# Performance work log

Hardware: AMD Instinct MI355X
Metric: run time of the kernel (lower is better)

The kernel has to match this reference:

```python
import jax, jax.numpy as jnp
import numpy as np

N = 4096      # num_nodes (single graph; batch is all-zeros in the original when absent)
CIN = 1024    # in_channels
H = 1024      # hidden_channels
COUT = 512    # out_channels
R = 10        # nodevec rank (hardcoded in the module)
BN_EPS = 1e-5


def setup_inputs() -> dict:
    key = jax.random.key(0)
    ks = jax.random.split(key, 8)
    w = lambda k, shp: jax.random.normal(k, shp, dtype=jnp.float32) * 0.02
    return {
        "x": jax.random.normal(ks[0], (N, CIN), dtype=jnp.float32),
        "w_map": w(ks[1], (CIN, H)),
        "b_map": jnp.zeros((H,), jnp.float32),
        "nv1": jax.random.normal(ks[2], (N, R), dtype=jnp.float32),
        "nv2": jax.random.normal(ks[3], (R, N), dtype=jnp.float32),
        "w1": w(ks[4], (H, H)),
        "b1": jnp.zeros((H,), jnp.float32),
        "w2": w(ks[5], (H, COUT)),
        "b2": jnp.zeros((COUT,), jnp.float32),
        "bn1_g": jnp.ones((H,), jnp.float32),
        "bn1_b": jnp.zeros((H,), jnp.float32),
        "bn1_m": jnp.zeros((H,), jnp.float32),
        "bn1_v": jnp.ones((H,), jnp.float32),
        "bn2_g": jnp.ones((COUT,), jnp.float32),
        "bn2_b": jnp.zeros((COUT,), jnp.float32),
        "bn2_m": jnp.zeros((COUT,), jnp.float32),
        "bn2_v": jnp.ones((COUT,), jnp.float32),
        "w_attn": w(ks[6], (COUT, 1)),
        "b_attn": jnp.zeros((1,), jnp.float32),
    }


def _batchnorm_eval(h, g, b, m, v):
    # BatchNorm1d in eval mode: running stats
    return (h - m) * jax.lax.rsqrt(v + BN_EPS) * g + b


def reference(x, w_map, b_map, nv1, nv2, w1, b1, w2, b2,
              bn1_g, bn1_b, bn1_m, bn1_v, bn2_g, bn2_b, bn2_m, bn2_v,
              w_attn, b_attn):
    # feature mapping
    xm = jax.nn.relu(x @ w_map + b_map)                       # [N, H]
    # adaptive adjacency: softmax(relu(nv1 @ nv2), dim=1) -> strictly positive,
    # so nonzero() yields the fully dense edge list; we keep it dense.
    adp = jax.nn.softmax(jax.nn.relu(nv1 @ nv2), axis=1)      # [N, N]
    # gcn_norm (PyG GCNConv default): add unit self-loops, normalize by
    # column-degree^-1/2 on both sides.
    A = adp + jnp.eye(N, dtype=adp.dtype)                      # [N, N]
    deg = jnp.sum(A, axis=0)                                   # column sums (target degree)
    dinv = jnp.where(deg > 0, jax.lax.rsqrt(deg), 0.0)
    An = (dinv[:, None] * A) * dinv[None, :]                   # D^-1/2 A D^-1/2
    # GCNConv: out_i = sum_j An[j, i] * (x W)_j + bias  =>  An^T @ (X W) + b
    h = jax.nn.relu(An.T @ (xm @ w1) + b1)                     # conv1 + relu
    h = _batchnorm_eval(h, bn1_g, bn1_b, bn1_m, bn1_v)         # bn1 (dropout off in eval)
    h = jax.nn.relu(An.T @ (h @ w2) + b2)                      # conv2 + relu
    h = _batchnorm_eval(h, bn2_g, bn2_b, bn2_m, bn2_v)         # bn2
    # global_mean_pool with batch == zeros -> single-graph mean
    pooled = jnp.mean(h, axis=0, keepdims=True)                # [1, COUT]
    attn = jax.nn.sigmoid(pooled @ w_attn + b_attn)            # [1, 1]
    return pooled * attn                                       # [1, COUT]
```

## Files before the change

kernel.cpp:

```cpp
#include <hip/hip_runtime.h>

#define NN 4096
#define R_RANK 10

typedef __bf16 bf16x8 __attribute__((ext_vector_type(8)));
typedef float floatx4 __attribute__((ext_vector_type(4)));

__device__ __forceinline__ unsigned short f2bf(float f) {
    union { float f; unsigned int u; } v; v.f = f;
    unsigned int r = v.u + 0x7FFFu + ((v.u >> 16) & 1u);
    return (unsigned short)(r >> 16);
}
__device__ __forceinline__ void gll16(const void* g, void* l) {
    __builtin_amdgcn_global_load_lds(
        (const __attribute__((address_space(1))) unsigned int*)g,
        (__attribute__((address_space(3))) unsigned int*)l, 16, 0, 0);
}

__global__ __launch_bounds__(256) void row_stats_kernel(
    const float* __restrict__ nv1, const float* __restrict__ nv2,
    float* __restrict__ rowmax, float* __restrict__ rowsum,
    float* __restrict__ deg, float* __restrict__ pooled)
{
    const int i0 = blockIdx.x * 4;
    const int tid = threadIdx.x;
    if (blockIdx.x < 16) deg[blockIdx.x * 256 + tid] = 0.f;
    if (blockIdx.x >= 16 && blockIdx.x < 18) pooled[(blockIdx.x - 16) * 256 + tid] = 0.f;
    __shared__ float a[4][R_RANK];
    if (tid < 4 * R_RANK) a[tid / R_RANK][tid % R_RANK] = nv1[i0 * R_RANK + tid];
    __syncthreads();

    float s[4][16];
    float mx[4] = {0.f, 0.f, 0.f, 0.f};
    #pragma unroll
    for (int t = 0; t < 16; ++t) {
        const int j = t * 256 + tid;
        float v[R_RANK];
        #pragma unroll
        for (int r = 0; r < R_RANK; ++r) v[r] = nv2[r * NN + j];
        #pragma unroll
        for (int q = 0; q < 4; ++q) {
            float acc = 0.f;
            #pragma unroll
            for (int r = 0; r < R_RANK; ++r) acc = fmaf(a[q][r], v[r], acc);
            acc = fmaxf(acc, 0.f);
            s[q][t] = acc;
            mx[q] = fmaxf(mx[q], acc);
        }
    }
    __shared__ float red[4][4];
    #pragma unroll
    for (int q = 0; q < 4; ++q) {
        float m = mx[q];
        #pragma unroll
        for (int off = 32; off > 0; off >>= 1) m = fmaxf(m, __shfl_down(m, off, 64));
        if ((tid & 63) == 0) red[q][tid >> 6] = m;
    }
    __syncthreads();
    #pragma unroll
    for (int q = 0; q < 4; ++q)
        mx[q] = fmaxf(fmaxf(red[q][0], red[q][1]), fmaxf(red[q][2], red[q][3]));
    __syncthreads();
    float sm[4] = {0.f, 0.f, 0.f, 0.f};
    #pragma unroll
    for (int t = 0; t < 16; ++t)
        #pragma unroll
        for (int q = 0; q < 4; ++q) sm[q] += __expf(s[q][t] - mx[q]);
    #pragma unroll
    for (int q = 0; q < 4; ++q) {
        float m = sm[q];
        #pragma unroll
        for (int off = 32; off > 0; off >>= 1) m += __shfl_down(m, off, 64);
        if ((tid & 63) == 0) red[q][tid >> 6] = m;
    }
    __syncthreads();
    if (tid < 4) {
        rowmax[i0 + tid] = mx[tid];
        rowsum[i0 + tid] = red[tid][0] + red[tid][1] + red[tid][2] + red[tid][3];
    }
}

__global__ __launch_bounds__(256) void col_sum_kernel(
    const float* __restrict__ nv1, const float* __restrict__ nv2,
    const float* __restrict__ rowmax, const float* __restrict__ rowsum,
    float* __restrict__ deg)
{
    const int j = blockIdx.x * 256 + threadIdx.x;
    const int i0 = blockIdx.y * 256;
    float v[R_RANK];
    #pragma unroll
    for (int r = 0; r < R_RANK; ++r) v[r] = nv2[r * NN + j];
    float acc = 0.f;
    for (int i = i0; i < i0 + 256; ++i) {
        float s = 0.f;
        #pragma unroll
        for (int r = 0; r < R_RANK; ++r) s = fmaf(nv1[i * R_RANK + r], v[r], s);
        s = fmaxf(s, 0.f);
        acc += __expf(s - rowmax[i]) * (1.0f / rowsum[i]);
    }
    atomicAdd(&deg[j], acc);
}

__global__ __launch_bounds__(256) void an_build_kernel(
    const float* __restrict__ nv1, const float* __restrict__ nv2,
    const float* __restrict__ rowmax, const float* __restrict__ rowsum,
    const float* __restrict__ deg, unsigned short* __restrict__ AnT)
{
    const int tid = threadIdx.x;
    const int j = blockIdx.x * 256 + tid;
    const int i0 = blockIdx.y * 8;
    __shared__ float v2s[8][R_RANK];
    __shared__ float dis[8];
    if (tid < 8 * R_RANK) {
        const int r = tid / 8, t = tid % 8;
        v2s[t][r] = nv2[r * NN + i0 + t];
    }
    if (tid < 8) dis[tid] = rsqrtf(1.0f + deg[i0 + tid]);

    float a[R_RANK];
    #pragma unroll
    for (int r = 0; r < R_RANK; ++r) a[r] = nv1[j * R_RANK + r];
    const float rm = rowmax[j];
    const float rs = 1.0f / rowsum[j];
    const float dj = rsqrtf(1.0f + deg[j]);
    __syncthreads();

    #pragma unroll
    for (int t = 0; t < 8; ++t) {
        const int i = i0 + t;
        float s = 0.f;
        #pragma unroll
        for (int r = 0; r < R_RANK; ++r) s = fmaf(a[r], v2s[t][r], s);
        s = fmaxf(s, 0.f);
        const float adp = __expf(s - rm) * rs;
        const float val = (adp + ((i == j) ? 1.f : 0.f)) * dis[t] * dj;
        AnT[(size_t)i * NN + j] = f2bf(val);
    }
}

__global__ __launch_bounds__(256) void prep_kernel(
    const float* __restrict__ x, const float* __restrict__ w_map,
    const float* __restrict__ w1, const float* __restrict__ w2,
    unsigned short* __restrict__ xb, unsigned short* __restrict__ wmT,
    unsigned short* __restrict__ w1T, unsigned short* __restrict__ w2T)
{
    const int z = blockIdx.z;
    const int tid = threadIdx.x;
    if (z == 3) {
        const int b = blockIdx.x + blockIdx.y * 32;
        const size_t base = (size_t)b * 4096 + (size_t)tid * 16;
        #pragma unroll
        for (int i = 0; i < 2; ++i) {
            const float4 a0 = *(const float4*)(x + base + i * 8);
            const float4 a1 = *(const float4*)(x + base + i * 8 + 4);
            ushort4 p, q;
            p.x = f2bf(a0.x); p.y = f2bf(a0.y); p.z = f2bf(a0.z); p.w = f2bf(a0.w);
            q.x = f2bf(a1.x); q.y = f2bf(a1.y); q.z = f2bf(a1.z); q.w = f2bf(a1.w);
            *(ushort4*)(xb + base + i * 8) = p;
            *(ushort4*)(xb + base + i * 8 + 4) = q;
        }
        return;
    }
    const float* W = (z == 0) ? w_map : (z == 1) ? w1 : w2;
    unsigned short* WT = (z == 0) ? wmT : (z == 1) ? w1T : w2T;
    const int CN = (z == 2) ? 512 : 1024;
    if (blockIdx.x * 32 >= CN) return;
    __shared__ float s[32][33];
    const int tx = tid & 31, ty = tid >> 5;
    const int r0 = blockIdx.y * 32, c0 = blockIdx.x * 32;
    #pragma unroll
    for (int i = 0; i < 4; ++i)
        s[ty + 8 * i][tx] = W[(size_t)(r0 + ty + 8 * i) * CN + c0 + tx];
    __syncthreads();
    #pragma unroll
    for (int i = 0; i < 4; ++i)
        WT[(size_t)(c0 + ty + 8 * i) * 1024 + r0 + tx] = f2bf(s[tx][ty + 8 * i]);
}

template<int OUTM, int EPI, int SK>
__global__ __launch_bounds__(512) void gemm_mfma(
    const unsigned short* __restrict__ A, const unsigned short* __restrict__ Bt,
    void* __restrict__ Out, const int M, const int N, const int K,
    const float* __restrict__ bias, const float* __restrict__ gamma,
    const float* __restrict__ beta, const float* __restrict__ mean,
    const float* __restrict__ var)
{
    __shared__ __align__(16) unsigned short As[4][8192];
    __shared__ __align__(16) unsigned short Bs[4][8192];
    const int tid = threadIdx.x;
    const int l = tid & 63, w = tid >> 6;
    const int wy = w >> 2, wx = w & 3;
    const int lr = l & 15, lq = l >> 4;

    const int gx = gridDim.x, gy = gridDim.y;
    int lin = blockIdx.x + gx * (blockIdx.y + gy * blockIdx.z);
    const int q = (gx * gy * gridDim.z) >> 3;
    lin = (lin & 7) * q + (lin >> 3);
    const int bx = lin % gx;
    const int by = (lin / gx) % gy;
    const int bz = lin / (gx * gy);

    const int row0 = by * 128, col0 = bx * 128;
    const int Kc = K / SK;
    const int kb = bz * Kc;
    const int nt = Kc >> 6;

    const unsigned short* Ag0 = A + (size_t)(row0 + w * 16 + lr) * K + kb + lq * 8;
    const unsigned short* Bg0 = Bt + (size_t)(col0 + w * 16 + lr) * K + kb + lq * 8;

    floatx4 acc[4][2];
    #pragma unroll
    for (int i = 0; i < 4; ++i)
        #pragma unroll
        for (int j = 0; j < 2; ++j) acc[i][j] = (floatx4){0.f, 0.f, 0.f, 0.f};

    #define STAGE(b, t)                                                         \
    {                                                                           \
        char* Aw = (char*)As[b] + w * 1024;                                     \
        char* Bw = (char*)Bs[b] + w * 1024;                                     \
        const int kk = (t) * 64;                                                \
        gll16(Ag0 + kk,      Aw);                                               \
        gll16(Ag0 + kk + 32, Aw + 8192);                                        \
        gll16(Bg0 + kk,      Bw);                                               \
        gll16(Bg0 + kk + 32, Bw + 8192);                                        \
    }

    STAGE(0, 0)
    STAGE(1, 1)
    const int nt2 = nt - 2;
    for (int t = 0; t < nt; ++t) {
        if (t < nt2) {
            STAGE((t + 2) & 3, t + 2)
            asm volatile("s_waitcnt vmcnt(8)" ::: "memory");
        } else if (t == nt2) {
            asm volatile("s_waitcnt vmcnt(4)" ::: "memory");
        } else {
            asm volatile("s_waitcnt vmcnt(0)" ::: "memory");
        }
        __builtin_amdgcn_sched_barrier(0);
        __builtin_amdgcn_s_barrier();
        __builtin_amdgcn_sched_barrier(0);

        const char* Afr = (const char*)As[t & 3] + wy * 4096 + l * 16;
        const char* Bfr = (const char*)Bs[t & 3] + wx * 2048 + l * 16;
        #pragma unroll
        for (int h = 0; h < 2; ++h) {
            bf16x8 af[4], bf[2];
            #pragma unroll
            for (int i = 0; i < 4; ++i) af[i] = *(const bf16x8*)(Afr + h * 8192 + i * 1024);
            #pragma unroll
            for (int j = 0; j < 2; ++j) bf[j] = *(const bf16x8*)(Bfr + h * 8192 + j * 1024);
            #pragma unroll
            for (int mf = 0; mf < 4; ++mf)
                #pragma unroll
                for (int nf = 0; nf < 2; ++nf)
                    acc[mf][nf] = __builtin_amdgcn_mfma_f32_16x16x32_bf16(
                        af[mf], bf[nf], acc[mf][nf], 0, 0, 0);
        }
    }
    #undef STAGE

    const int gr0 = row0 + wy * 64 + lq * 4;
    const int gc0 = col0 + wx * 32 + lr;
    if constexpr (OUTM == 0) {
        float* Pz = (float*)Out + (size_t)bz * M * N;
        #pragma unroll
        for (int mf = 0; mf < 4; ++mf) {
            const int gr = gr0 + mf * 16;
            #pragma unroll
            for (int nf = 0; nf < 2; ++nf) {
                const int gc = gc0 + nf * 16;
                #pragma unroll
                for (int r = 0; r < 4; ++r)
                    Pz[(size_t)(gr + r) * N + gc] = acc[mf][nf][r];
            }
        }
    } else if constexpr (OUTM == 1) {
        unsigned short* O = (unsigned short*)Out;
        #pragma unroll
        for (int nf = 0; nf < 2; ++nf) {
            const int gc = gc0 + nf * 16;
            float bb = 0.f, sc = 1.f, sh = 0.f;
            if constexpr (EPI >= 1) bb = bias[gc];
            if constexpr (EPI == 2) {
                sc = gamma[gc] * rsqrtf(var[gc] + 1e-5f);
                sh = beta[gc] - mean[gc] * sc;
            }
            #pragma unroll
            for (int mf = 0; mf < 4; ++mf) {
                const int gr = gr0 + mf * 16;
                #pragma unroll
                for (int r = 0; r < 4; ++r) {
                    float xv = acc[mf][nf][r];
                    if constexpr (EPI >= 1) xv = fmaxf(xv + bb, 0.f);
                    if constexpr (EPI == 2) xv = fmaf(xv, sc, sh);
                    O[(size_t)(gr + r) * N + gc] = f2bf(xv);
                }
            }
        }
    } else {
        unsigned short* O = (unsigned short*)Out;
        #pragma unroll
        for (int mf = 0; mf < 4; ++mf) {
            const int gr = gr0 + mf * 16;
            #pragma unroll
            for (int nf = 0; nf < 2; ++nf) {
                const int gc = gc0 + nf * 16;
                ushort4 p;
                p.x = f2bf(acc[mf][nf][0]); p.y = f2bf(acc[mf][nf][1]);
                p.z = f2bf(acc[mf][nf][2]); p.w = f2bf(acc[mf][nf][3]);
                *(ushort4*)&O[(size_t)gc * M + gr] = p;
            }
        }
    }
}

template<int EPI, int S, int NC>
__global__ __launch_bounds__(256) void reduce_k(
    const float* __restrict__ P, unsigned short* __restrict__ out, const int MN,
    const float* __restrict__ bias, const float* __restrict__ gamma,
    const float* __restrict__ beta, const float* __restrict__ mean,
    const float* __restrict__ var)
{
    const int idx = blockIdx.x * 256 + threadIdx.x;
    const int n4 = MN >> 2;
    const float4* Pv = (const float4*)P;
    float4 v = Pv[idx];
    #pragma unroll
    for (int z = 1; z < S; ++z) {
        const float4 t = Pv[idx + (size_t)z * n4];
        v.x += t.x; v.y += t.y; v.z += t.z; v.w += t.w;
    }
    float vals[4] = {v.x, v.y, v.z, v.w};
    if constexpr (EPI >= 1) {
        const int c0 = (idx << 2) & (NC - 1);
        const float4 b4 = *(const float4*)(bias + c0);
        const float bb[4] = {b4.x, b4.y, b4.z, b4.w};
        float sc[4], sh[4];
        if constexpr (EPI == 2) {
            const float4 g4 = *(const float4*)(gamma + c0);
            const float4 e4 = *(const float4*)(beta + c0);
            const float4 m4 = *(const float4*)(mean + c0);
            const float4 v4 = *(const float4*)(var + c0);
            const float gg[4] = {g4.x, g4.y, g4.z, g4.w};
            const float ee[4] = {e4.x, e4.y, e4.z, e4.w};
            const float mm[4] = {m4.x, m4.y, m4.z, m4.w};
            const float vv[4] = {v4.x, v4.y, v4.z, v4.w};
            #pragma unroll
            for (int j = 0; j < 4; ++j) {
                sc[j] = gg[j] * rsqrtf(vv[j] + 1e-5f);
                sh[j] = ee[j] - mm[j] * sc[j];
            }
        }
        #pragma unroll
        for (int j = 0; j < 4; ++j) {
            float xv = fmaxf(vals[j] + bb[j], 0.f);
            if constexpr (EPI == 2) xv = fmaf(xv, sc[j], sh[j]);
            vals[j] = xv;
        }
    }
    ushort4 p;
    p.x = f2bf(vals[0]); p.y = f2bf(vals[1]); p.z = f2bf(vals[2]); p.w = f2bf(vals[3]);
    *(ushort4*)(out + ((size_t)idx << 2)) = p;
}

template<int S>
__global__ __launch_bounds__(256) void reduce_pool_kernel(
    const float* __restrict__ P, float* __restrict__ pooled,
    const float* __restrict__ bias, const float* __restrict__ gamma,
    const float* __restrict__ beta, const float* __restrict__ mean,
    const float* __restrict__ var)
{
    const int idx = blockIdx.x * 256 + threadIdx.x;
    const int row = blockIdx.x >> 2;
    constexpr int n4 = 512 * 4096 / 4;
    const float4* Pv = (const float4*)P;
    float4 v = Pv[idx];
    #pragma unroll
    for (int z = 1; z < S; ++z) {
        const float4 t = Pv[idx + (size_t)z * n4];
        v.x += t.x; v.y += t.y; v.z += t.z; v.w += t.w;
    }
    const float b0 = bias[row];
    const float sc = gamma[row] * rsqrtf(var[row] + 1e-5f);
    const float sh = beta[row] - mean[row] * sc;
    float s = 0.f;
    const float vals[4] = {v.x, v.y, v.z, v.w};
    #pragma unroll
    for (int j = 0; j < 4; ++j)
        s += fmaf(fmaxf(vals[j] + b0, 0.f), sc, sh);
    #pragma unroll
    for (int off = 32; off > 0; off >>= 1) s += __shfl_down(s, off, 64);
    __shared__ float red[4];
    if ((threadIdx.x & 63) == 0) red[threadIdx.x >> 6] = s;
    __syncthreads();
    if (threadIdx.x == 0)
        atomicAdd(&pooled[row], red[0] + red[1] + red[2] + red[3]);
}

__global__ __launch_bounds__(512) void finalize_kernel(
    const float* __restrict__ pooled, const float* __restrict__ w_attn,
    const float* __restrict__ b_attn, float* __restrict__ out)
{
    const int c = threadIdx.x;
    __shared__ float red[512];
    const float p = pooled[c] * (1.0f / 4096.0f);
    red[c] = p * w_attn[c];
    __syncthreads();
    for (int s = 256; s > 0; s >>= 1) {
        if (c < s) red[c] += red[c + s];
        __syncthreads();
    }
    const float attn = 1.0f / (1.0f + __expf(-(red[0] + b_attn[0])));
    out[c] = p * attn;
}

extern "C" void kernel_launch(void* const* d_in, const int* in_sizes, int n_in,
                              void* d_out, int out_size, void* d_ws, size_t ws_size,
                              hipStream_t stream) {
    const float* x      = (const float*)d_in[0];
    const float* w_map  = (const float*)d_in[1];
    const float* b_map  = (const float*)d_in[2];
    const float* nv1    = (const float*)d_in[3];
    const float* nv2    = (const float*)d_in[4];
    const float* w1     = (const float*)d_in[5];
    const float* b1     = (const float*)d_in[6];
    const float* w2     = (const float*)d_in[7];
    const float* b2     = (const float*)d_in[8];
    const float* bn1_g  = (const float*)d_in[9];
    const float* bn1_b  = (const float*)d_in[10];
    const float* bn1_m  = (const float*)d_in[11];
    const float* bn1_v  = (const float*)d_in[12];
    const float* bn2_g  = (const float*)d_in[13];
    const float* bn2_b  = (const float*)d_in[14];
    const float* bn2_m  = (const float*)d_in[15];
    const float* bn2_v  = (const float*)d_in[16];
    const float* w_attn = (const float*)d_in[17];
    const float* b_attn = (const float*)d_in[18];
    float* out = (float*)d_out;

    const size_t MB = 1024 * 1024;
    char* ws = (char*)d_ws;
    unsigned short* AnT = (unsigned short*)(ws);
    float*          P   = (float*)(ws + 32 * MB);
    char* B0 = ws + 64 * MB;
    unsigned short* xb  = (unsigned short*)(B0);
    unsigned short* t1T = (unsigned short*)(B0);
    unsigned short* t2T = (unsigned short*)(B0);
    unsigned short* xm  = (unsigned short*)(B0 + 8 * MB);
    unsigned short* h1  = (unsigned short*)(B0 + 8 * MB);
    unsigned short* wmT = (unsigned short*)(B0 + 16 * MB);
    unsigned short* w1T = (unsigned short*)(B0 + 18 * MB);
    unsigned short* w2T = (unsigned short*)(B0 + 20 * MB);
    float* deg    = (float*)(B0 + 21 * MB);
    float* rowmax = deg + 4096;
    float* rowsum = rowmax + 4096;
    float* pooled = rowsum + 4096;

    prep_kernel<<<dim3(32, 32, 4), 256, 0, stream>>>(x, w_map, w1, w2, xb, wmT, w1T, w2T);
    row_stats_kernel<<<1024, 256, 0, stream>>>(nv1, nv2, rowmax, rowsum, deg, pooled);
    col_sum_kernel<<<dim3(16, 16), 256, 0, stream>>>(nv1, nv2, rowmax, rowsum, deg);
    an_build_kernel<<<dim3(16, 512), 256, 0, stream>>>(nv1, nv2, rowmax, rowsum, deg, AnT);

    gemm_mfma<1, 1, 1><<<dim3(8, 32, 1), 512, 0, stream>>>(xb, wmT, xm,
        4096, 1024, 1024, b_map, nullptr, nullptr, nullptr, nullptr);
    gemm_mfma<2, 0, 1><<<dim3(8, 32, 1), 512, 0, stream>>>(xm, w1T, t1T,
        4096, 1024, 1024, nullptr, nullptr, nullptr, nullptr, nullptr);
    gemm_mfma<1, 2, 1><<<dim3(8, 32, 1), 512, 0, stream>>>(AnT, t1T, h1,
        4096, 1024, 4096, b1, bn1_g, bn1_b, bn1_m, bn1_v);
    gemm_mfma<0, 0, 2><<<dim3(32, 4, 2), 512, 0, stream>>>(w2T, h1, P,
        512, 4096, 1024, nullptr, nullptr, nullptr, nullptr, nullptr);
    reduce_k<0, 2, 1><<<2048, 256, 0, stream>>>(P, t2T, 2097152,
        nullptr, nullptr, nullptr, nullptr, nullptr);
    gemm_mfma<0, 0, 2><<<dim3(32, 4, 2), 512, 0, stream>>>(t2T, AnT, P,
        512, 4096, 4096, nullptr, nullptr, nullptr, nullptr, nullptr);
    reduce_pool_kernel<2><<<2048, 256, 0, stream>>>(
        P, pooled, b2, bn2_g, bn2_b, bn2_m, bn2_v);

    finalize_kernel<<<1, 512, 0, stream>>>(pooled, w_attn, b_attn, out);
}
```

Before: 356.3 us.

## Add 256x256-tile split-K MFMA GEMM for the adjacency aggregations

Adds a new bf16 MFMA GEMM kernel with 256x256 output tiles, a 64-wide K step, double-buffered LDS loads via global_load_lds, a remapped block order and split-K partials written as fp32. Both An^T aggregation GEMMs now use it, followed by reduce kernels that apply bias, ReLU and batchnorm (or pooling) over the partials. The xm@w1 GEMM is recast to produce the transposed output directly instead of using a transposed-store epilogue. The larger tiles raise data reuse per block and split-K keeps the grid filled. The cost is extra fp32 partial traffic and reduction passes, plus a workspace-size-dependent choice between 4-way and 2-way split.

Result: slower. 368.0 us (+3.3%).

```diff
diff --git a/kernel.cpp b/kernel.cpp
--- a/kernel.cpp
+++ b/kernel.cpp
@@ -275,7 +275,7 @@
                     Pz[(size_t)(gr + r) * N + gc] = acc[mf][nf][r];
             }
         }
-    } else if constexpr (OUTM == 1) {
+    } else {
         unsigned short* O = (unsigned short*)Out;
         #pragma unroll
         for (int nf = 0; nf < 2; ++nf) {
@@ -298,19 +298,108 @@
                 }
             }
         }
-    } else {
-        unsigned short* O = (unsigned short*)Out;
-        #pragma unroll
-        for (int mf = 0; mf < 4; ++mf) {
-            const int gr = gr0 + mf * 16;
-            #pragma unroll
-            for (int nf = 0; nf < 2; ++nf) {
-                const int gc = gc0 + nf * 16;
-                ushort4 p;
-                p.x = f2bf(acc[mf][nf][0]); p.y = f2bf(acc[mf][nf][1]);
-                p.z = f2bf(acc[mf][nf][2]); p.w = f2bf(acc[mf][nf][3]);
-                *(ushort4*)&O[(size_t)gc * M + gr] = p;
-            }
+    }
+}
+
+template<int SK>
+__global__ __launch_bounds__(512, 2) void gemm_mfma256(
+    const unsigned short* __restrict__ A, const unsigned short* __restrict__ Bt,
+    float* __restrict__ P, const int M, const int N, const int K)
+{
+    __shared__ __align__(16) unsigned short L[2][32768];
+    const int tid = threadIdx.x;
+    const int l = tid & 63, w = tid >> 6;
+    const int wy = w >> 2, wx = w & 3;
+    const int lr = l & 15, lq = l >> 4;
+    (void)lr; (void)lq;
+
+    const int gx = gridDim.x, gy = gridDim.y;
+    int lin = blockIdx.x + gx * (blockIdx.y + gy * blockIdx.z);
+    const int q = (gx * gy * gridDim.z) >> 3;
+    lin = (lin & 7) * q + (lin >> 3);
+    const int bx = lin % gx;
+    const int by = (lin / gx) % gy;
+    const int bz = lin / (gx * gy);
+
+    const int row0 = by * 256, col0 = bx * 256;
+    const int Kc = K / SK, kb = bz * Kc;
+    const int nt = Kc >> 6;
+
+    const unsigned short* Ag0 = A + (size_t)(row0 + 32 * w + (l & 15)) * K + kb + (l >> 4) * 8;
+    const unsigned short* Ag1 = Ag0 + (size_t)16 * K;
+    const unsigned short* Bg0 = Bt + (size_t)(col0 + 32 * w + (l & 15)) * K + kb + (l >> 4) * 8;
+    const unsigned short* Bg1 = Bg0 + (size_t)16 * K;
+
+    floatx4 acc[8][4];
+    #pragma unroll
+    for (int i = 0; i < 8; ++i)
+        #pragma unroll
+        for (int j = 0; j < 4; ++j) acc[i][j] = (floatx4){0.f, 0.f, 0.f, 0.f};
+
+    #define STAGE256(b, t)                                                      \
+    {                                                                           \
+        char* Ld = (char*)L[b] + w * 2048;                                      \
+        const int kk = (t) * 64;                                                \
+        gll16(Ag0 + kk,      Ld);                                               \
+        gll16(Ag1 + kk,      Ld + 1024);                                        \
+        gll16(Ag0 + kk + 32, Ld + 16384);                                       \
+        gll16(Ag1 + kk + 32, Ld + 16384 + 1024);                                \
+        gll16(Bg0 + kk,      Ld + 32768);                                       \
+        gll16(Bg1 + kk,      Ld + 32768 + 1024);                                \
+        gll16(Bg0 + kk + 32, Ld + 32768 + 16384);                               \
+        gll16(Bg1 + kk + 32, Ld + 32768 + 16384 + 1024);                        \
+    }
+
+    STAGE256(0, 0)
+    int cur = 0;
+    for (int t = 0; t < nt; ++t) {
+        if (t + 1 < nt) {
+            STAGE256(cur ^ 1, t + 1)
+            asm volatile("s_waitcnt vmcnt(8)" ::: "memory");
+        } else {
+            asm volatile("s_waitcnt vmcnt(0)" ::: "memory");
+        }
+        __builtin_amdgcn_sched_barrier(0);
+        __builtin_amdgcn_s_barrier();
+        __builtin_amdgcn_sched_barrier(0);
+
+        const char* Ab = (const char*)L[cur] + wy * 8192 + l * 16;
+        const char* Bb = (const char*)L[cur] + 32768 + wx * 4096 + l * 16;
+        #pragma unroll
+        for (int h = 0; h < 2; ++h) {
+            bf16x8 af[8], bf[4];
+            #pragma unroll
+            for (int i = 0; i < 8; ++i) af[i] = *(const bf16x8*)(Ab + h * 16384 + i * 1024);
+            #pragma unroll
+            for (int j = 0; j < 4; ++j) bf[j] = *(const bf16x8*)(Bb + h * 16384 + j * 1024);
+            __builtin_amdgcn_s_setprio(1);
+            #pragma unroll
+            for (int mf = 0; mf < 8; ++mf)
+                #pragma unroll
+                for (int nf = 0; nf < 4; ++nf)
+                    acc[mf][nf] = __builtin_amdgcn_mfma_f32_16x16x32_bf16(
+                        af[mf], bf[nf], acc[mf][nf], 0, 0, 0);
+            __builtin_amdgcn_s_setprio(0);
+        }
+        __builtin_amdgcn_sched_barrier(0);
+        __builtin_amdgcn_s_barrier();
+        __builtin_amdgcn_sched_barrier(0);
+        cur ^= 1;
+    }
+    #undef STAGE256
+
+    float* Pz = P + (size_t)bz * M * N;
+    const int gr0 = row0 + wy * 128 + (l >> 4) * 4;
+    const int gc0 = col0 + wx * 64 + (l & 15);
+    #pragma unroll
+    for (int mf = 0; mf < 8; ++mf) {
+        const int gr = gr0 + mf * 16;
+        #pragma unroll
+        for (int nf = 0; nf < 4; ++nf) {
+            const int gc = gc0 + nf * 16;
+            #pragma unroll
+            for (int r = 0; r < 4; ++r)
+                Pz[(size_t)(gr + r) * N + gc] = acc[mf][nf][r];
         }
     }
 }
@@ -440,10 +529,11 @@
     float* out = (float*)d_out;
 
     const size_t MB = 1024 * 1024;
+    const bool big = ws_size >= 118 * MB;
     char* ws = (char*)d_ws;
     unsigned short* AnT = (unsigned short*)(ws);
     float*          P   = (float*)(ws + 32 * MB);
-    char* B0 = ws + 64 * MB;
+    char* B0 = big ? (ws + 96 * MB) : (ws + 64 * MB);
     unsigned short* xb  = (unsigned short*)(B0);
     unsigned short* t1T = (unsigned short*)(B0);
     unsigned short* t2T = (unsigned short*)(B0);
@@ -464,17 +554,23 @@
 
     gemm_mfma<1, 1, 1><<<dim3(8, 32, 1), 512, 0, stream>>>(xb, wmT, xm,
         4096, 1024, 1024, b_map, nullptr, nullptr, nullptr, nullptr);
-    gemm_mfma<2, 0, 1><<<dim3(8, 32, 1), 512, 0, stream>>>(xm, w1T, t1T,
-        4096, 1024, 1024, nullptr, nullptr, nullptr, nullptr, nullptr);
-    gemm_mfma<1, 2, 1><<<dim3(8, 32, 1), 512, 0, stream>>>(AnT, t1T, h1,
-        4096, 1024, 4096, b1, bn1_g, bn1_b, bn1_m, bn1_v);
+    gemm_mfma<1, 0, 1><<<dim3(32, 8, 1), 512, 0, stream>>>(w1T, xm, t1T,
+        1024, 4096, 1024, nullptr, nullptr, nullptr, nullptr, nullptr);
+    if (big) {
+        gemm_mfma256<4><<<dim3(4, 16, 4), 512, 0, stream>>>(AnT, t1T, P, 4096, 1024, 4096);
+        reduce_k<2, 4, 1024><<<4096, 256, 0, stream>>>(P, h1, 4194304,
+            b1, bn1_g, bn1_b, bn1_m, bn1_v);
+    } else {
+        gemm_mfma256<2><<<dim3(4, 16, 2), 512, 0, stream>>>(AnT, t1T, P, 4096, 1024, 4096);
+        reduce_k<2, 2, 1024><<<4096, 256, 0, stream>>>(P, h1, 4194304,
+            b1, bn1_g, bn1_b, bn1_m, bn1_v);
+    }
     gemm_mfma<0, 0, 2><<<dim3(32, 4, 2), 512, 0, stream>>>(w2T, h1, P,
         512, 4096, 1024, nullptr, nullptr, nullptr, nullptr, nullptr);
     reduce_k<0, 2, 1><<<2048, 256, 0, stream>>>(P, t2T, 2097152,
         nullptr, nullptr, nullptr, nullptr, nullptr);
-    gemm_mfma<0, 0, 2><<<dim3(32, 4, 2), 512, 0, stream>>>(t2T, AnT, P,
-        512, 4096, 4096, nullptr, nullptr, nullptr, nullptr, nullptr);
-    reduce_pool_kernel<2><<<2048, 256, 0, stream>>>(
+    gemm_mfma256<4><<<dim3(16, 2, 4), 512, 0, stream>>>(t2T, AnT, P, 512, 4096, 4096);
+    reduce_pool_kernel<4><<<2048, 256, 0, stream>>>(
         P, pooled, b2, bn2_g, bn2_b, bn2_m, bn2_v);
 
     finalize_kernel<<<1, 512, 0, stream>>>(pooled, w_attn, b_attn, out);
```
